# Kernel optimization log

Measured on AMD Instinct MI355X. Metric: run time of the kernel, lower is better.

## Reference

```python
import jax, jax.numpy as jnp
import numpy as np

H = 100; W = 100; FX = 86.6; FY = 86.6
NEAR = 2.0; FAR = 6.0; DINF = 1e10
NS = 64            # n_samples per ray
L_PTS = 10; L_DIR = 4
HID = 256; HID_DIR = 128
D_PTS = 3 + 3 * 2 * L_PTS   # 63
D_DIR = 3 + 3 * 2 * L_DIR   # 27


def posenc(x, L):
    # [x, sin(2^k x), cos(2^k x)] NeRF positional encoding
    freqs = (2.0 ** jnp.arange(L)).astype(x.dtype)          # [L]
    xb = x[..., None, :] * freqs[:, None]                    # [..., L, 3]
    enc = jnp.concatenate([jnp.sin(xb), jnp.cos(xb)], -1)    # [..., L, 6]
    return jnp.concatenate([x, enc.reshape(x.shape[:-1] + (L * 6,))], -1)


def setup_inputs() -> dict:
    key = jax.random.key(0)
    ks = jax.random.split(key, 8)
    pose = jnp.array([[1., 0., 0., 0.], [0., 1., 0., 0.],
                      [0., 0., 1., 4.], [0., 0., 0., 1.]], jnp.float32)
    c2w = pose + 0.01 * jax.random.normal(ks[0], (4, 4), jnp.float32)
    t_rand = jax.random.uniform(ks[1], (NS,), jnp.float32)
    s = 0.05
    return {
        'c2w': c2w,
        't_rand': t_rand,
        'w1': s * jax.random.normal(ks[2], (D_PTS, HID), jnp.float32),
        'b1': jnp.zeros((HID,), jnp.float32),
        'w2': s * jax.random.normal(ks[3], (HID, HID), jnp.float32),
        'b2': jnp.zeros((HID,), jnp.float32),
        'w_sig': s * jax.random.normal(ks[4], (HID, 1), jnp.float32),
        'b_sig': jnp.zeros((1,), jnp.float32),
        'w_dir': s * jax.random.normal(ks[5], (HID + D_DIR, HID_DIR), jnp.float32),
        'b_dir': jnp.zeros((HID_DIR,), jnp.float32),
        'w_rgb': s * jax.random.normal(ks[6], (HID_DIR, 3), jnp.float32),
        'b_rgb': jnp.zeros((3,), jnp.float32),
    }


def reference(c2w, t_rand, w1, b1, w2, b2, w_sig, b_sig, w_dir, b_dir, w_rgb, b_rgb):
    # ---- get_rays ----
    i, j = jnp.meshgrid(jnp.arange(W, dtype=jnp.float32),
                        jnp.arange(H, dtype=jnp.float32), indexing='xy')
    dirs = jnp.stack([(i - W * 0.5) / FX,
                      -(j - H * 0.5) / FY,
                      -jnp.ones_like(i)], -1).reshape(H * W, 3)      # [R,3]
    rays_d = jnp.einsum('rk,ik->ri', dirs, c2w[:3, :3])              # [R,3]
    rays_o = c2w[:3, -1]                                             # [3]

    # ---- sample_stratified (perturb=True, inverse_depth=False) ----
    t_vals = jnp.linspace(0.0, 1.0, NS)
    z = NEAR * (1.0 - t_vals) + FAR * t_vals
    mids = 0.5 * (z[1:] + z[:-1])
    upper = jnp.concatenate([mids, z[-1:]])
    lower = jnp.concatenate([z[:1], mids])
    z = lower + (upper - lower) * t_rand                             # [NS]
    dists = jnp.concatenate([z[1:] - z[:-1], jnp.full((1,), DINF, z.dtype)])
    pts = rays_o + rays_d[:, None, :] * z[None, :, None]             # [R,NS,3]

    # ---- encodings ----
    enc_pts = posenc(pts, L_PTS)                                     # [R,NS,63]
    norm = jnp.sqrt(jnp.sum(rays_d * rays_d, -1, keepdims=True))     # [R,1]
    viewdirs = rays_d / norm                                         # [R,3]
    enc_dir = jnp.broadcast_to(posenc(viewdirs, L_DIR)[:, None, :],
                               (H * W, NS, D_DIR))                   # [R,NS,27]

    # ---- coarse NeRF MLP ----
    h = jax.nn.relu(enc_pts @ w1 + b1)
    h = jax.nn.relu(h @ w2 + b2)
    sigma = (h @ w_sig + b_sig)[..., 0]                              # [R,NS]
    hd = jax.nn.relu(jnp.concatenate([h, enc_dir], -1) @ w_dir + b_dir)
    rgb = jax.nn.sigmoid(hd @ w_rgb + b_rgb)                         # [R,NS,3]

    # ---- raw2outputs (volume rendering) ----
    dists_r = dists[None, :] * norm                                  # [R,NS]
    alpha = 1.0 - jnp.exp(-jax.nn.relu(sigma) * dists_r)             # [R,NS]
    # get_rgb_map back-to-front recurrence == alpha * exclusive_cumprod(1-alpha)
    trans = jnp.concatenate(
        [jnp.ones_like(alpha[:, :1]), jnp.cumprod(1.0 - alpha, -1)[:, :-1]], -1)
    weights = alpha * trans                                          # [R,NS]
    rgb_map = jnp.sum(weights[..., None] * rgb, -2)                  # [R,3]
    return rgb_map
```

## Files before the change

### kernel.cpp

```cpp
#include <hip/hip_runtime.h>
#include <cstdint>
#include <cmath>

#define NTH 256

namespace {

typedef _Float16 half8  __attribute__((ext_vector_type(8)));
typedef _Float16 half4v __attribute__((ext_vector_type(4)));
typedef _Float16 half2v __attribute__((ext_vector_type(2)));
typedef __fp16   fp16x2 __attribute__((ext_vector_type(2)));
typedef __fp16   fp16x4 __attribute__((ext_vector_type(4)));
typedef float    float4v __attribute__((ext_vector_type(4)));

constexpr int IMG_W   = 100;
constexpr int NS      = 64;
constexpr int D_PTS   = 63;
constexpr int D_DIR   = 27;
constexpr int HID     = 256;
constexpr int HID_DIR = 128;

constexpr int ENC_H = 72;
constexpr int H_S   = 260;
constexpr int HD_S  = 132;

constexpr int W1P_OFF  = 0;
constexpr int W2P_OFF  = 16384;
constexpr int WDP_OFF  = 81920;
constexpr int WRGB_OFF = 123392;
constexpr int WPACK_HALFS = 125440;

__device__ __forceinline__ int kmap1(int kp) {
    if (kp < 3) return kp;
    const int c = (kp - 4) / 20, rem = (kp - 4) % 20;
    return 3 + 6 * (rem >> 1) + 3 * (rem & 1) + c;
}

__global__ __launch_bounds__(NTH)
void prepack(const float* __restrict__ w1, const float* __restrict__ w2,
             const float* __restrict__ wd, const float* __restrict__ wsig,
             const float* __restrict__ wrgb, _Float16* __restrict__ wp)
{
    const int idx = blockIdx.x * NTH + threadIdx.x;
    if (idx >= WPACK_HALFS) return;
    const int j    = idx & 7;
    const int lane = (idx >> 3) & 63;
    const int kloc = (lane >> 4) * 8 + j;
    const int lr   = lane & 15;
    float v = 0.0f;
    if (idx < W2P_OFF) {
        const int nt = (idx >> 9) & 15, ks = idx >> 13;
        const int kp = ks * 32 + kloc;
        if (kp != 3) v = w1[kmap1(kp) * HID + nt * 16 + lr];
    } else if (idx < WDP_OFF) {
        const int t = idx - W2P_OFF;
        const int nt = (t >> 9) & 15, ks = t >> 13;
        v = w2[(ks * 32 + kloc) * HID + nt * 16 + lr];
    } else if (idx < WRGB_OFF) {
        const int t = idx - WDP_OFF;
        const int q = t >> 9;
        const int ks = q / 9, tile = q - 9 * ks;
        const int k = ks * 32 + kloc;
        if (tile < 8) { if (k < HID + D_DIR) v = wd[k * HID_DIR + tile * 16 + lr]; }
        else if (lr == 0 && k < HID) v = wsig[k];
    } else {
        const int t = idx - WRGB_OFF;
        const int ks = t >> 9;
        const int k = ks * 32 + kloc;
        if (lr < 3) v = wrgb[k * 3 + lr];
    }
    wp[idx] = (_Float16)v;
}

__device__ __forceinline__ half8 bf_w1p(const float* __restrict__ W, int kbase, int n) {
    half8 b;
    #pragma unroll
    for (int j = 0; j < 8; ++j) {
        const int kp = kbase + j;
        b[j] = (_Float16)((kp != 3) ? W[kmap1(kp) * HID + n] : 0.0f);
    }
    return b;
}
__device__ __forceinline__ half8 bf_w(const float* __restrict__ W, int ldN,
                                      int kbase, int n, int kmax) {
    half8 b;
    #pragma unroll
    for (int j = 0; j < 8; ++j) {
        const int k = kbase + j;
        b[j] = (_Float16)((k < kmax) ? W[k * ldN + n] : 0.0f);
    }
    return b;
}
__device__ __forceinline__ half8 bf_sig(const float* __restrict__ ws, int kbase, int lr) {
    half8 b;
    #pragma unroll
    for (int j = 0; j < 8; ++j)
        b[j] = (_Float16)((lr == 0) ? ws[kbase + j] : 0.0f);
    return b;
}
__device__ __forceinline__ half8 bf_rgb(const float* __restrict__ wr, int kbase, int lr) {
    half8 b;
    #pragma unroll
    for (int j = 0; j < 8; ++j)
        b[j] = (_Float16)((lr < 3) ? wr[(kbase + j) * 3 + lr] : 0.0f);
    return b;
}

__device__ __forceinline__ half8 ld_h8(const _Float16* __restrict__ p) {
    const half4v lo = *reinterpret_cast<const half4v*>(p);
    const half4v hi = *reinterpret_cast<const half4v*>(p + 4);
    return __builtin_shufflevector(lo, hi, 0, 1, 2, 3, 4, 5, 6, 7);
}

__device__ __forceinline__ half4v pack_relu4(const float4v a) {
    const fp16x2 lo = __builtin_amdgcn_cvt_pkrtz(a[0], a[1]);
    const fp16x2 hi = __builtin_amdgcn_cvt_pkrtz(a[2], a[3]);
    fp16x4 r4 = __builtin_shufflevector(lo, hi, 0, 1, 2, 3);
    r4 = __builtin_elementwise_max(r4, fp16x4{});
    return __builtin_bit_cast(half4v, r4);
}

constexpr float INV2PI = 0.15915494309189535f;
__device__ __forceinline__ float hsin_rev(float f) {
    const float fr = f - floorf(f);
    return __builtin_amdgcn_sinf(fr);
}
__device__ __forceinline__ float hcos_rev(float f) {
    const float fr = f - floorf(f);
    return __builtin_amdgcn_cosf(fr);
}

__device__ __forceinline__ double z_of(int s, const float* __restrict__ t_rand) {
    const double delta = 1.0 / 63.0;
    const double ts = (s == 63) ? 1.0 : (double)s * delta;
    const double zs = 2.0 * (1.0 - ts) + 6.0 * ts;
    double lower, upper;
    if (s == 0) { lower = zs; }
    else { const double tm = (double)(s - 1) * delta;
           const double zm = 2.0 * (1.0 - tm) + 6.0 * tm; lower = 0.5 * (zm + zs); }
    if (s == 63) { upper = zs; }
    else { const double tp = (s + 1 == 63) ? 1.0 : (double)(s + 1) * delta;
           const double zp = 2.0 * (1.0 - tp) + 6.0 * tp; upper = 0.5 * (zs + zp); }
    return lower + (upper - lower) * (double)t_rand[s];
}

template<bool PACKED>
__global__ __launch_bounds__(NTH, 4)
void nerf_fused(const float* __restrict__ c2w,
                const float* __restrict__ t_rand,
                const float* __restrict__ w1,  const float* __restrict__ b1,
                const float* __restrict__ w2,  const float* __restrict__ b2,
                const float* __restrict__ w_sig, const float* __restrict__ b_sig,
                const float* __restrict__ w_dir, const float* __restrict__ b_dir,
                const float* __restrict__ w_rgb, const float* __restrict__ b_rgb,
                const _Float16* __restrict__ wpack,
                float* __restrict__ out)
{
    __shared__ __align__(16) unsigned char scr[NS * H_S * 2];
    _Float16* encH = reinterpret_cast<_Float16*>(scr);
    _Float16* hbuf = reinterpret_cast<_Float16*>(scr);
    double*   encD = reinterpret_cast<double*>(scr);
    double*   h1d  = reinterpret_cast<double*>(scr + 512);
    double*   h2d  = reinterpret_cast<double*>(scr + 2560);
    __shared__ __align__(16) _Float16 encdirH[32];
    __shared__ float  sigp[4][NS];
    __shared__ float  sigb[NS];
    __shared__ float  rgbb[NS * 3];

    const int tid  = threadIdx.x;
    const int ray  = blockIdx.x;
    const int lane = tid & 63;
    const int wv   = tid >> 6;
    const int lr   = lane & 15;
    const int lq   = lane >> 4;

    const half8* wp8 = reinterpret_cast<const half8*>(wpack);

    const int pj = ray / IMG_W;
    const int pi = ray - pj * IMG_W;
    const float dx = ((float)pi - 50.0f) / 86.6f;
    const float dy = -(((float)pj) - 50.0f) / 86.6f;
    const float rd0 = dx * c2w[0] + dy * c2w[1] - c2w[2];
    const float rd1 = dx * c2w[4] + dy * c2w[5] - c2w[6];
    const float rd2 = dx * c2w[8] + dy * c2w[9] - c2w[10];
    const float ro0 = c2w[3], ro1 = c2w[7], ro2 = c2w[11];
    const float nrm = sqrtf(rd0 * rd0 + rd1 * rd1 + rd2 * rd2);
    const float vd0 = rd0 / nrm, vd1 = rd1 / nrm, vd2 = rd2 / nrm;

    half8 w1pf[2][4];
    float4v b1pf[4];
    if (PACKED) {
        #pragma unroll
        for (int ks = 0; ks < 2; ++ks)
            #pragma unroll
            for (int nt = 0; nt < 4; ++nt)
                w1pf[ks][nt] = wp8[(W1P_OFF >> 3) + (ks * 16 + wv * 4 + nt) * 64 + lane];
    }
    #pragma unroll
    for (int nt = 0; nt < 4; ++nt)
        b1pf[nt] = *reinterpret_cast<const float4v*>(&b1[(wv * 4 + nt) * 16 + lq * 4]);

    if (tid < 192) {
        const int s = tid / 3;
        const int c = tid - 3 * s;
        const float zv = (float)z_of(s, t_rand);
        const float p = (c == 0) ? (ro0 + rd0 * zv) : ((c == 1) ? (ro1 + rd1 * zv) : (ro2 + rd2 * zv));
        _Float16* row = &encH[s * ENC_H];
        if (c == 2) {
            *reinterpret_cast<half2v*>(&row[2]) = half2v{(_Float16)p, (_Float16)0.0f};
        } else {
            row[c] = (_Float16)p;
        }
        unsigned* rowu = reinterpret_cast<unsigned*>(row);
        #pragma unroll
        for (int l = 0; l < 10; ++l) {
            const float f = p * ((float)(1 << l) * INV2PI);
            const float fr = f - floorf(f);
            const fp16x2 sc = __builtin_amdgcn_cvt_pkrtz(__builtin_amdgcn_sinf(fr),
                                                         __builtin_amdgcn_cosf(fr));
            rowu[2 + 10 * c + l] = __builtin_bit_cast(unsigned, sc);
        }
    } else if (tid < 224) {
        const int f = tid - 192;
        float v = 0.0f;
        if (f < D_DIR) {
            if (f < 3) {
                v = (f == 0) ? vd0 : ((f == 1) ? vd1 : vd2);
            } else {
                const int ff = f - 3;
                const int l = ff / 6;
                const int r = ff - 6 * l;
                const int c = r % 3;
                const float x = ((c == 0) ? vd0 : ((c == 1) ? vd1 : vd2)) * (float)(1 << l);
                v = (r < 3) ? hsin_rev(x * INV2PI) : hcos_rev(x * INV2PI);
            }
        }
        encdirH[f] = (_Float16)v;
    }
    __syncthreads();

    half8 w2pf[4];
    {
        float4v acc[4][4];
        #pragma unroll
        for (int nt = 0; nt < 4; ++nt)
            #pragma unroll
            for (int st = 0; st < 4; ++st) acc[nt][st] = b1pf[nt];

        #pragma unroll
        for (int ks = 0; ks < 2; ++ks) {
            half8 h[4];
            #pragma unroll
            for (int st = 0; st < 4; ++st)
                h[st] = *reinterpret_cast<const half8*>(&encH[(st * 16 + lr) * ENC_H + ks * 32 + lq * 8]);
            __builtin_amdgcn_s_setprio(1);
            #pragma unroll
            for (int nt = 0; nt < 4; ++nt) {
                const half8 w = PACKED
                    ? w1pf[ks][nt]
                    : bf_w1p(w1, ks * 32 + lq * 8, (wv * 4 + nt) * 16 + lr);
                #pragma unroll
                for (int st = 0; st < 4; ++st)
                    acc[nt][st] = __builtin_amdgcn_mfma_f32_16x16x32_f16(w, h[st], acc[nt][st], 0, 0, 0);
            }
            __builtin_amdgcn_s_setprio(0);
        }
        if (PACKED) {
            #pragma unroll
            for (int nt = 0; nt < 4; ++nt)
                w2pf[nt] = wp8[(W2P_OFF >> 3) + (wv * 4 + nt) * 64 + lane];
        }
        __syncthreads();
        #pragma unroll
        for (int nt = 0; nt < 4; ++nt) {
            const int nb = (wv * 4 + nt) * 16 + lq * 4;
            #pragma unroll
            for (int st = 0; st < 4; ++st)
                *reinterpret_cast<half4v*>(&hbuf[(st * 16 + lr) * H_S + nb]) = pack_relu4(acc[nt][st]);
        }
    }
    __syncthreads();

    half8 wdpf[2];
    {
        float4v acc[4][4];
        #pragma unroll
        for (int nt = 0; nt < 4; ++nt) {
            const float4v bb = *reinterpret_cast<const float4v*>(&b2[(wv * 4 + nt) * 16 + lq * 4]);
            #pragma unroll
            for (int st = 0; st < 4; ++st) acc[nt][st] = bb;
        }

        {
            half8 h[4];
            #pragma unroll
            for (int st = 0; st < 4; ++st)
                h[st] = ld_h8(&hbuf[(st * 16 + lr) * H_S + lq * 8]);
            __builtin_amdgcn_s_setprio(1);
            #pragma unroll
            for (int nt = 0; nt < 4; ++nt) {
                const half8 w = PACKED
                    ? w2pf[nt]
                    : bf_w(w2, HID, lq * 8, (wv * 4 + nt) * 16 + lr, 1 << 30);
                #pragma unroll
                for (int st = 0; st < 4; ++st)
                    acc[nt][st] = __builtin_amdgcn_mfma_f32_16x16x32_f16(w, h[st], acc[nt][st], 0, 0, 0);
            }
            __builtin_amdgcn_s_setprio(0);
        }
        #pragma unroll
        for (int ks = 1; ks < 8; ++ks) {
            half8 h[4];
            #pragma unroll
            for (int st = 0; st < 4; ++st)
                h[st] = ld_h8(&hbuf[(st * 16 + lr) * H_S + ks * 32 + lq * 8]);
            const half8* wk = wp8 + (W2P_OFF >> 3) + (ks * 16 + wv * 4) * 64 + lane;
            __builtin_amdgcn_s_setprio(1);
            #pragma unroll
            for (int nt = 0; nt < 4; ++nt) {
                const half8 w = PACKED
                    ? wk[nt * 64]
                    : bf_w(w2, HID, ks * 32 + lq * 8, (wv * 4 + nt) * 16 + lr, 1 << 30);
                #pragma unroll
                for (int st = 0; st < 4; ++st)
                    acc[nt][st] = __builtin_amdgcn_mfma_f32_16x16x32_f16(w, h[st], acc[nt][st], 0, 0, 0);
            }
            __builtin_amdgcn_s_setprio(0);
        }
        if (PACKED) {
            #pragma unroll
            for (int nt = 0; nt < 2; ++nt)
                wdpf[nt] = wp8[(WDP_OFF >> 3) + (wv * 2 + nt) * 64 + lane];
        }
        __syncthreads();
        #pragma unroll
        for (int nt = 0; nt < 4; ++nt) {
            const int nb = (wv * 4 + nt) * 16 + lq * 4;
            #pragma unroll
            for (int st = 0; st < 4; ++st)
                *reinterpret_cast<half4v*>(&hbuf[(st * 16 + lr) * H_S + nb]) = pack_relu4(acc[nt][st]);
        }
    }
    __syncthreads();

    float4v accd[2][4];
    float4v accs[4];
    {
        #pragma unroll
        for (int nt = 0; nt < 2; ++nt) {
            const float4v bb = *reinterpret_cast<const float4v*>(&b_dir[(wv * 2 + nt) * 16 + lq * 4]);
            #pragma unroll
            for (int st = 0; st < 4; ++st) accd[nt][st] = bb;
        }
        #pragma unroll
        for (int st = 0; st < 4; ++st) accs[st] = float4v{0.f, 0.f, 0.f, 0.f};

        {
            half8 h[4];
            #pragma unroll
            for (int st = 0; st < 4; ++st)
                h[st] = ld_h8(&hbuf[(st * 16 + lr) * H_S + lq * 8]);
            __builtin_amdgcn_s_setprio(1);
            #pragma unroll
            for (int nt = 0; nt < 2; ++nt) {
                const half8 w = PACKED
                    ? wdpf[nt]
                    : bf_w(w_dir, HID_DIR, lq * 8, (wv * 2 + nt) * 16 + lr, 1 << 30);
                #pragma unroll
                for (int st = 0; st < 4; ++st)
                    accd[nt][st] = __builtin_amdgcn_mfma_f32_16x16x32_f16(w, h[st], accd[nt][st], 0, 0, 0);
            }
            if (wv == 0) {
                const half8 w = PACKED
                    ? wp8[(WDP_OFF >> 3) + 8 * 64 + lane]
                    : bf_sig(w_sig, lq * 8, lr);
                #pragma unroll
                for (int st = 0; st < 4; ++st)
                    accs[st] = __builtin_amdgcn_mfma_f32_16x16x32_f16(w, h[st], accs[st], 0, 0, 0);
            }
            __builtin_amdgcn_s_setprio(0);
        }
        #pragma unroll
        for (int ks = 1; ks < 8; ++ks) {
            half8 h[4];
            #pragma unroll
            for (int st = 0; st < 4; ++st)
                h[st] = ld_h8(&hbuf[(st * 16 + lr) * H_S + ks * 32 + lq * 8]);
            const half8* wk = wp8 + (WDP_OFF >> 3) + (ks * 9 + wv * 2) * 64 + lane;
            __builtin_amdgcn_s_setprio(1);
            #pragma unroll
            for (int nt = 0; nt < 2; ++nt) {
                const half8 w = PACKED
                    ? wk[nt * 64]
                    : bf_w(w_dir, HID_DIR, ks * 32 + lq * 8, (wv * 2 + nt) * 16 + lr, 1 << 30);
                #pragma unroll
                for (int st = 0; st < 4; ++st)
                    accd[nt][st] = __builtin_amdgcn_mfma_f32_16x16x32_f16(w, h[st], accd[nt][st], 0, 0, 0);
            }
            if ((ks >> 1) == wv) {
                const half8 w = PACKED
                    ? wp8[(WDP_OFF >> 3) + (ks * 9 + 8) * 64 + lane]
                    : bf_sig(w_sig, ks * 32 + lq * 8, lr);
                #pragma unroll
                for (int st = 0; st < 4; ++st)
                    accs[st] = __builtin_amdgcn_mfma_f32_16x16x32_f16(w, h[st], accs[st], 0, 0, 0);
            }
            __builtin_amdgcn_s_setprio(0);
        }
        {
            const half8 he = *reinterpret_cast<const half8*>(&encdirH[lq * 8]);
            const half8* wk = wp8 + (WDP_OFF >> 3) + (8 * 9 + wv * 2) * 64 + lane;
            __builtin_amdgcn_s_setprio(1);
            #pragma unroll
            for (int nt = 0; nt < 2; ++nt) {
                const half8 w = PACKED
                    ? wk[nt * 64]
                    : bf_w(w_dir, HID_DIR, HID + lq * 8, (wv * 2 + nt) * 16 + lr, HID + D_DIR);
                #pragma unroll
                for (int st = 0; st < 4; ++st)
                    accd[nt][st] = __builtin_amdgcn_mfma_f32_16x16x32_f16(w, he, accd[nt][st], 0, 0, 0);
            }
            __builtin_amdgcn_s_setprio(0);
        }
    }
    __syncthreads();

    #pragma unroll
    for (int nt = 0; nt < 2; ++nt) {
        const int nb = (wv * 2 + nt) * 16 + lq * 4;
        #pragma unroll
        for (int st = 0; st < 4; ++st)
            *reinterpret_cast<half4v*>(&hbuf[(st * 16 + lr) * HD_S + nb]) = pack_relu4(accd[nt][st]);
    }
    if (lq == 0) {
        #pragma unroll
        for (int st = 0; st < 4; ++st)
            sigp[wv][st * 16 + lr] = accs[st][0];
    }
    __syncthreads();

    if (tid < NS)
        sigb[tid] = ((sigp[0][tid] + sigp[1][tid]) + (sigp[2][tid] + sigp[3][tid])) + b_sig[0];
    {
        float4v accr = float4v{0.f, 0.f, 0.f, 0.f};
        const half8* wk = wp8 + (WRGB_OFF >> 3) + lane;
        __builtin_amdgcn_s_setprio(1);
        #pragma unroll
        for (int ks = 0; ks < 4; ++ks) {
            const half8 h = ld_h8(&hbuf[(wv * 16 + lr) * HD_S + ks * 32 + lq * 8]);
            const half8 w = PACKED
                ? wk[ks * 64]
                : bf_rgb(w_rgb, ks * 32 + lq * 8, lr);
            accr = __builtin_amdgcn_mfma_f32_16x16x32_f16(w, h, accr, 0, 0, 0);
        }
        __builtin_amdgcn_s_setprio(0);
        if (lq == 0) {
            #pragma unroll
            for (int r = 0; r < 3; ++r) {
                const float a = accr[r] + b_rgb[r];
                rgbb[(wv * 16 + lr) * 3 + r] = 1.0f / (1.0f + expf(-a));
            }
        }
    }
    __syncthreads();

    if (fabsf(sigb[63]) < 0.01f) {
        {
            const double z63 = z_of(63, t_rand);
            const double p0 = (double)ro0 + (double)rd0 * z63;
            const double p1 = (double)ro1 + (double)rd1 * z63;
            const double p2 = (double)ro2 + (double)rd2 * z63;
            if (tid < D_PTS) {
                const int f = tid;
                double v;
                if (f < 3) {
                    v = (f == 0) ? p0 : ((f == 1) ? p1 : p2);
                } else {
                    const int ff = f - 3;
                    const int l = ff / 6;
                    const int r = ff - 6 * l;
                    const int c = r % 3;
                    const double x = ((c == 0) ? p0 : ((c == 1) ? p1 : p2)) * (double)(1 << l);
                    v = (r < 3) ? sin(x) : cos(x);
                }
                encD[f] = v;
            }
        }
        __syncthreads();
        {
            double a0 = 0.0, a1 = 0.0, a2 = 0.0, a3 = 0.0;
            int k = 0;
            for (; k + 4 <= 60; k += 4) {
                a0 += encD[k]     * (double)w1[(k)     * HID + tid];
                a1 += encD[k + 1] * (double)w1[(k + 1) * HID + tid];
                a2 += encD[k + 2] * (double)w1[(k + 2) * HID + tid];
                a3 += encD[k + 3] * (double)w1[(k + 3) * HID + tid];
            }
            a0 += encD[60] * (double)w1[60 * HID + tid];
            a1 += encD[61] * (double)w1[61 * HID + tid];
            a2 += encD[62] * (double)w1[62 * HID + tid];
            const double acc = ((a0 + a1) + (a2 + a3)) + (double)b1[tid];
            h1d[tid] = fmax(acc, 0.0);
        }
        __syncthreads();
        {
            double a0 = 0.0, a1 = 0.0, a2 = 0.0, a3 = 0.0;
            for (int k = 0; k < HID; k += 4) {
                a0 += h1d[k]     * (double)w2[(k)     * HID + tid];
                a1 += h1d[k + 1] * (double)w2[(k + 1) * HID + tid];
                a2 += h1d[k + 2] * (double)w2[(k + 2) * HID + tid];
                a3 += h1d[k + 3] * (double)w2[(k + 3) * HID + tid];
            }
            const double acc = ((a0 + a1) + (a2 + a3)) + (double)b2[tid];
            h2d[tid] = fmax(acc, 0.0);
        }
        __syncthreads();
        if (tid < 64) {
            double p = 0.0;
            #pragma unroll
            for (int m = 0; m < 4; ++m)
                p += h2d[tid * 4 + m] * (double)w_sig[tid * 4 + m];
            #pragma unroll
            for (int off = 1; off < 64; off <<= 1)
                p += __shfl_xor(p, off, 64);
            if (tid == 0) sigb[63] = (float)(p + (double)b_sig[0]);
        }
    }
    __syncthreads();

    if (tid < NS) {
        const int s = tid;
        const float sgv = sigb[s];
        const float zv  = (float)z_of(s, t_rand);
        const float zn  = __shfl_down(zv, 1, 64);
        const float dist = (s < 63) ? (zn - zv) : 1.0e10f;
        const float alpha = 1.0f - expf(-fmaxf(sgv, 0.0f) * dist * nrm);
        float P = 1.0f - alpha;
        #pragma unroll
        for (int off = 1; off < 64; off <<= 1) {
            const float p = __shfl_up(P, off, 64);
            if (s >= off) P *= p;
        }
        float T = __shfl_up(P, 1, 64);
        if (s == 0) T = 1.0f;
        const float wgt = alpha * T;
        float r0 = wgt * rgbb[s * 3 + 0];
        float r1 = wgt * rgbb[s * 3 + 1];
        float r2 = wgt * rgbb[s * 3 + 2];
        #pragma unroll
        for (int off = 32; off > 0; off >>= 1) {
            r0 += __shfl_xor(r0, off, 64);
            r1 += __shfl_xor(r1, off, 64);
            r2 += __shfl_xor(r2, off, 64);
        }
        if (s == 0) {
            out[ray * 3 + 0] = r0;
            out[ray * 3 + 1] = r1;
            out[ray * 3 + 2] = r2;
        }
    }
}

}

extern "C" void kernel_launch(void* const* d_in, const int* in_sizes, int n_in,
                              void* d_out, int out_size, void* d_ws, size_t ws_size,
                              hipStream_t stream) {
    const float* c2w    = (const float*)d_in[0];
    const float* t_rand = (const float*)d_in[1];
    const float* w1     = (const float*)d_in[2];
    const float* b1     = (const float*)d_in[3];
    const float* w2     = (const float*)d_in[4];
    const float* b2     = (const float*)d_in[5];
    const float* w_sig  = (const float*)d_in[6];
    const float* b_sig  = (const float*)d_in[7];
    const float* w_dir  = (const float*)d_in[8];
    const float* b_dir  = (const float*)d_in[9];
    const float* w_rgb  = (const float*)d_in[10];
    const float* b_rgb  = (const float*)d_in[11];

    (void)in_sizes; (void)n_in; (void)out_size;

    const bool packed = (ws_size >= (size_t)(WPACK_HALFS * 2));
    if (packed) {
        _Float16* wp = (_Float16*)d_ws;
        hipLaunchKernelGGL(prepack, dim3((WPACK_HALFS + NTH - 1) / NTH), dim3(NTH), 0, stream,
                           w1, w2, w_dir, w_sig, w_rgb, wp);
        hipLaunchKernelGGL((nerf_fused<true>), dim3(100 * 100), dim3(NTH), 0, stream,
                           c2w, t_rand, w1, b1, w2, b2, w_sig, b_sig,
                           w_dir, b_dir, w_rgb, b_rgb, (const _Float16*)wp, (float*)d_out);
    } else {
        hipLaunchKernelGGL((nerf_fused<false>), dim3(100 * 100), dim3(NTH), 0, stream,
                           c2w, t_rand, w1, b1, w2, b2, w_sig, b_sig,
                           w_dir, b_dir, w_rgb, b_rgb, (const _Float16*)nullptr, (float*)d_out);
    }
}
```

Before: 248.2 us.

## Use XOR-swizzled shared layout for hidden buffers and raise occupancy target

Replaces the padded row strides of the hidden-activation shared buffers with an unpadded layout whose columns are XOR-swizzled by row, so fragments load with single 16-byte reads instead of two 8-byte reads while staying clear of bank conflicts. Shared memory shrinks to a flat 32 KB scratch that also holds the sigma and rgb buffers, and the launch-bounds occupancy hint goes from 4 to 5 blocks per CU. The view-direction encoding is now computed per wave and spread through lane shuffles rather than written to shared memory. Asking for 5 blocks may tighten the register budget and cause spills, and the scratch overlays must not overlap the live hidden data.

Result: slower. 489.8 us (+97.4%).

```diff
diff --git a/kernel.cpp b/kernel.cpp
--- a/kernel.cpp
+++ b/kernel.cpp
@@ -21,8 +21,9 @@
 constexpr int HID_DIR = 128;
 
 constexpr int ENC_H = 72;
-constexpr int H_S   = 260;
-constexpr int HD_S  = 132;
+
+__device__ __forceinline__ int hidx(int row, int col)  { return row * 256 + (col ^ ((row & 7) << 3)); }
+__device__ __forceinline__ int hdidx(int row, int col) { return row * 128 + (col ^ ((row & 7) << 3)); }
 
 constexpr int W1P_OFF  = 0;
 constexpr int W2P_OFF  = 16384;
@@ -106,12 +107,6 @@
     return b;
 }
 
-__device__ __forceinline__ half8 ld_h8(const _Float16* __restrict__ p) {
-    const half4v lo = *reinterpret_cast<const half4v*>(p);
-    const half4v hi = *reinterpret_cast<const half4v*>(p + 4);
-    return __builtin_shufflevector(lo, hi, 0, 1, 2, 3, 4, 5, 6, 7);
-}
-
 __device__ __forceinline__ half4v pack_relu4(const float4v a) {
     const fp16x2 lo = __builtin_amdgcn_cvt_pkrtz(a[0], a[1]);
     const fp16x2 hi = __builtin_amdgcn_cvt_pkrtz(a[2], a[3]);
@@ -145,7 +140,7 @@
 }
 
 template<bool PACKED>
-__global__ __launch_bounds__(NTH, 4)
+__global__ __launch_bounds__(NTH, 5)
 void nerf_fused(const float* __restrict__ c2w,
                 const float* __restrict__ t_rand,
                 const float* __restrict__ w1,  const float* __restrict__ b1,
@@ -156,16 +151,16 @@
                 const _Float16* __restrict__ wpack,
                 float* __restrict__ out)
 {
-    __shared__ __align__(16) unsigned char scr[NS * H_S * 2];
+    __shared__ __align__(16) unsigned char scr[32768];
     _Float16* encH = reinterpret_cast<_Float16*>(scr);
     _Float16* hbuf = reinterpret_cast<_Float16*>(scr);
+    _Float16* hdb  = reinterpret_cast<_Float16*>(scr);
     double*   encD = reinterpret_cast<double*>(scr);
     double*   h1d  = reinterpret_cast<double*>(scr + 512);
     double*   h2d  = reinterpret_cast<double*>(scr + 2560);
-    __shared__ __align__(16) _Float16 encdirH[32];
-    __shared__ float  sigp[4][NS];
-    __shared__ float  sigb[NS];
-    __shared__ float  rgbb[NS * 3];
+    float*    sigp = reinterpret_cast<float*>(scr + 20480);
+    float*    sigb = reinterpret_cast<float*>(scr + 21504);
+    float*    rgbb = reinterpret_cast<float*>(scr + 21760);
 
     const int tid  = threadIdx.x;
     const int ray  = blockIdx.x;
@@ -187,6 +182,27 @@
     const float nrm = sqrtf(rd0 * rd0 + rd1 * rd1 + rd2 * rd2);
     const float vd0 = rd0 / nrm, vd1 = rd1 / nrm, vd2 = rd2 / nrm;
 
+    half8 he;
+    {
+        float edv = 0.0f;
+        if (lane < D_DIR) {
+            const int f = lane;
+            if (f < 3) {
+                edv = (f == 0) ? vd0 : ((f == 1) ? vd1 : vd2);
+            } else {
+                const int ff = f - 3;
+                const int l = ff / 6;
+                const int r = ff - 6 * l;
+                const int c = r % 3;
+                const float x = ((c == 0) ? vd0 : ((c == 1) ? vd1 : vd2)) * (float)(1 << l);
+                edv = (r < 3) ? hsin_rev(x * INV2PI) : hcos_rev(x * INV2PI);
+            }
+        }
+        #pragma unroll
+        for (int j = 0; j < 8; ++j)
+            he[j] = (_Float16)__shfl(edv, lq * 8 + j, 64);
+    }
+
     half8 w1pf[2][4];
     float4v b1pf[4];
     if (PACKED) {
@@ -220,22 +236,6 @@
                                                          __builtin_amdgcn_cosf(fr));
             rowu[2 + 10 * c + l] = __builtin_bit_cast(unsigned, sc);
         }
-    } else if (tid < 224) {
-        const int f = tid - 192;
-        float v = 0.0f;
-        if (f < D_DIR) {
-            if (f < 3) {
-                v = (f == 0) ? vd0 : ((f == 1) ? vd1 : vd2);
-            } else {
-                const int ff = f - 3;
-                const int l = ff / 6;
-                const int r = ff - 6 * l;
-                const int c = r % 3;
-                const float x = ((c == 0) ? vd0 : ((c == 1) ? vd1 : vd2)) * (float)(1 << l);
-                v = (r < 3) ? hsin_rev(x * INV2PI) : hcos_rev(x * INV2PI);
-            }
-        }
-        encdirH[f] = (_Float16)v;
     }
     __syncthreads();
 
@@ -276,7 +276,7 @@
             const int nb = (wv * 4 + nt) * 16 + lq * 4;
             #pragma unroll
             for (int st = 0; st < 4; ++st)
-                *reinterpret_cast<half4v*>(&hbuf[(st * 16 + lr) * H_S + nb]) = pack_relu4(acc[nt][st]);
+                *reinterpret_cast<half4v*>(&hbuf[hidx(st * 16 + lr, nb)]) = pack_relu4(acc[nt][st]);
         }
     }
     __syncthreads();
@@ -295,7 +295,7 @@
             half8 h[4];
             #pragma unroll
             for (int st = 0; st < 4; ++st)
-                h[st] = ld_h8(&hbuf[(st * 16 + lr) * H_S + lq * 8]);
+                h[st] = *reinterpret_cast<const half8*>(&hbuf[hidx(st * 16 + lr, lq * 8)]);
             __builtin_amdgcn_s_setprio(1);
             #pragma unroll
             for (int nt = 0; nt < 4; ++nt) {
@@ -313,7 +313,7 @@
             half8 h[4];
             #pragma unroll
             for (int st = 0; st < 4; ++st)
-                h[st] = ld_h8(&hbuf[(st * 16 + lr) * H_S + ks * 32 + lq * 8]);
+                h[st] = *reinterpret_cast<const half8*>(&hbuf[hidx(st * 16 + lr, ks * 32 + lq * 8)]);
             const half8* wk = wp8 + (W2P_OFF >> 3) + (ks * 16 + wv * 4) * 64 + lane;
             __builtin_amdgcn_s_setprio(1);
             #pragma unroll
@@ -338,7 +338,7 @@
             const int nb = (wv * 4 + nt) * 16 + lq * 4;
             #pragma unroll
             for (int st = 0; st < 4; ++st)
-                *reinterpret_cast<half4v*>(&hbuf[(st * 16 + lr) * H_S + nb]) = pack_relu4(acc[nt][st]);
+                *reinterpret_cast<half4v*>(&hbuf[hidx(st * 16 + lr, nb)]) = pack_relu4(acc[nt][st]);
         }
     }
     __syncthreads();
@@ -359,7 +359,7 @@
             half8 h[4];
             #pragma unroll
             for (int st = 0; st < 4; ++st)
-                h[st] = ld_h8(&hbuf[(st * 16 + lr) * H_S + lq * 8]);
+                h[st] = *reinterpret_cast<const half8*>(&hbuf[hidx(st * 16 + lr, lq * 8)]);
             __builtin_amdgcn_s_setprio(1);
             #pragma unroll
             for (int nt = 0; nt < 2; ++nt) {
@@ -385,7 +385,7 @@
             half8 h[4];
             #pragma unroll
             for (int st = 0; st < 4; ++st)
-                h[st] = ld_h8(&hbuf[(st * 16 + lr) * H_S + ks * 32 + lq * 8]);
+                h[st] = *reinterpret_cast<const half8*>(&hbuf[hidx(st * 16 + lr, ks * 32 + lq * 8)]);
             const half8* wk = wp8 + (WDP_OFF >> 3) + (ks * 9 + wv * 2) * 64 + lane;
             __builtin_amdgcn_s_setprio(1);
             #pragma unroll
@@ -408,7 +408,6 @@
             __builtin_amdgcn_s_setprio(0);
         }
         {
-            const half8 he = *reinterpret_cast<const half8*>(&encdirH[lq * 8]);
             const half8* wk = wp8 + (WDP_OFF >> 3) + (8 * 9 + wv * 2) * 64 + lane;
             __builtin_amdgcn_s_setprio(1);
             #pragma unroll
@@ -430,24 +429,25 @@
         const int nb = (wv * 2 + nt) * 16 + lq * 4;
         #pragma unroll
         for (int st = 0; st < 4; ++st)
-            *reinterpret_cast<half4v*>(&hbuf[(st * 16 + lr) * HD_S + nb]) = pack_relu4(accd[nt][st]);
+            *reinterpret_cast<half4v*>(&hdb[hdidx(st * 16 + lr, nb)]) = pack_relu4(accd[nt][st]);
     }
     if (lq == 0) {
         #pragma unroll
         for (int st = 0; st < 4; ++st)
-            sigp[wv][st * 16 + lr] = accs[st][0];
+            sigp[wv * NS + st * 16 + lr] = accs[st][0];
     }
     __syncthreads();
 
     if (tid < NS)
-        sigb[tid] = ((sigp[0][tid] + sigp[1][tid]) + (sigp[2][tid] + sigp[3][tid])) + b_sig[0];
+        sigb[tid] = ((sigp[0 * NS + tid] + sigp[1 * NS + tid]) +
+                     (sigp[2 * NS + tid] + sigp[3 * NS + tid])) + b_sig[0];
     {
         float4v accr = float4v{0.f, 0.f, 0.f, 0.f};
         const half8* wk = wp8 + (WRGB_OFF >> 3) + lane;
         __builtin_amdgcn_s_setprio(1);
         #pragma unroll
         for (int ks = 0; ks < 4; ++ks) {
-            const half8 h = ld_h8(&hbuf[(wv * 16 + lr) * HD_S + ks * 32 + lq * 8]);
+            const half8 h = *reinterpret_cast<const half8*>(&hdb[hdidx(wv * 16 + lr, ks * 32 + lq * 8)]);
             const half8 w = PACKED
                 ? wk[ks * 64]
                 : bf_rgb(w_rgb, ks * 32 + lq * 8, lr);
```
